# Kernel optimization log

Hardware: AMD Instinct MI355X
Metric: run time of the kernel (lower is better)

## Reference

```python
import jax, jax.numpy as jnp
import numpy as np
import math

B, SQ, SKV, H = 8, 1024, 1024, 1024
NH, HD = 16, 64  # num_attention_heads, attention_head_size


def setup_inputs() -> dict:
    key = jax.random.key(0)
    ks = jax.random.split(key, 6)
    s = 1.0 / math.sqrt(H)
    return {
        "hidden_states": jax.random.normal(ks[0], (B, SQ, H), jnp.float32),
        "keyvalue_states": jax.random.normal(ks[1], (B, SKV, H), jnp.float32),
        "attention_mask": jnp.zeros((B, 1, 1, SKV), jnp.float32),
        "Wq": jax.random.normal(ks[2], (H, H), jnp.float32) * s,
        "bq": jnp.zeros((H,), jnp.float32),
        "Wk": jax.random.normal(ks[3], (H, H), jnp.float32) * s,
        "bk": jnp.zeros((H,), jnp.float32),
        "Wv": jax.random.normal(ks[4], (H, H), jnp.float32) * s,
        "bv": jnp.zeros((H,), jnp.float32),
    }


def _split_heads(x):
    # [B, S, H] -> [B, NH, S, HD]
    b, s, _ = x.shape
    return x.reshape(b, s, NH, HD).transpose(0, 2, 1, 3)


def reference(hidden_states, keyvalue_states, attention_mask, Wq, bq, Wk, bk, Wv, bv):
    q = _split_heads(hidden_states @ Wq.T + bq)     # [B, NH, SQ, HD]
    k = _split_heads(keyvalue_states @ Wk.T + bk)   # [B, NH, SKV, HD]
    v = _split_heads(keyvalue_states @ Wv.T + bv)   # [B, NH, SKV, HD]
    scores = jnp.einsum("bhqd,bhkd->bhqk", q, k) / math.sqrt(HD)
    scores = scores + attention_mask                 # additive mask broadcast
    probs = jax.nn.softmax(scores, axis=-1)          # dropout = identity (eval)
    ctx = jnp.einsum("bhqk,bhkd->bhqd", probs, v)
    ctx = ctx.transpose(0, 2, 1, 3).reshape(hidden_states.shape[0], -1, NH * HD)
    return ctx
```

## Files before the change

### kernel.cpp

```cpp
#include <hip/hip_runtime.h>
#include <hip/hip_bf16.h>


typedef __attribute__((ext_vector_type(8))) short short8;
typedef __attribute__((ext_vector_type(4))) short short4v;
typedef __attribute__((ext_vector_type(4))) float f32x4;
typedef __attribute__((ext_vector_type(2))) float f32x2;
typedef __attribute__((ext_vector_type(16))) float f32x16;
typedef __attribute__((ext_vector_type(2))) unsigned uint2v;
typedef __attribute__((ext_vector_type(4))) int int4v;

#define AS1(p) ((const __attribute__((address_space(1))) void*)(p))
#define AS3(p) ((__attribute__((address_space(3))) void*)(p))

__device__ inline short f2bs(float x) {
    __hip_bfloat16 h = __float2bfloat16(x);
    return *reinterpret_cast<short*>(&h);
}

__global__ __launch_bounds__(256) void cvt_bf16(
    const float* __restrict__ s0, const float* __restrict__ s1,
    const float* __restrict__ s2, const float* __restrict__ s3,
    const float* __restrict__ s4,
    short* __restrict__ d0, short* __restrict__ d1,
    short* __restrict__ d2, short* __restrict__ d3, short* __restrict__ d4)
{
    const float* s; short* d; int n4;
    switch (blockIdx.y) {
        case 0: s = s0; d = d0; n4 = 2097152; break;
        case 1: s = s1; d = d1; n4 = 2097152; break;
        case 2: s = s2; d = d2; n4 = 262144;  break;
        case 3: s = s3; d = d3; n4 = 262144;  break;
        default: s = s4; d = d4; n4 = 262144; break;
    }
    for (int i = blockIdx.x * 256 + threadIdx.x; i < n4; i += gridDim.x * 256) {
        float4 v = ((const float4*)s)[i];
        short4v o;
        o.x = f2bs(v.x); o.y = f2bs(v.y); o.z = f2bs(v.z); o.w = f2bs(v.w);
        ((short4v*)d)[i] = o;
    }
}

__global__ __launch_bounds__(256) void qkv_gemm(
    const short* __restrict__ hsb, const short* __restrict__ kvb,
    const short* __restrict__ wqb, const short* __restrict__ wkb,
    const short* __restrict__ wvb,
    const float* __restrict__ bq, const float* __restrict__ bk,
    const float* __restrict__ bv,
    short* __restrict__ qo, short* __restrict__ ko, short* __restrict__ vo)
{
    const short* A; const short* W; const float* bias; short* dst;
    int z = blockIdx.z;
    if (z == 0)      { A = hsb; W = wqb; bias = bq; dst = qo; }
    else if (z == 1) { A = kvb; W = wkb; bias = bk; dst = ko; }
    else             { A = kvb; W = wvb; bias = bv; dst = vo; }

    __shared__ __align__(16) short As[128 * 64];
    __shared__ __align__(16) short Bs[128 * 64];

    const int t = threadIdx.x;
    const int lane = t & 63;
    const int wave = t >> 6;
    const int lane31 = lane & 31;
    const int hi = lane >> 5;
    const int wm = (wave & 1) * 64;
    const int wn = (wave >> 1) * 64;
    const int m0 = blockIdx.x * 128;
    const int n0 = blockIdx.y * 128;

    f32x16 acc[2][2] = {};

    for (int k0 = 0; k0 < 1024; k0 += 64) {
        #pragma unroll
        for (int i = 0; i < 4; ++i) {
            int c = i * 256 + t;
            int row = c >> 3;
            int gc = (c & 7) ^ (row & 7);
            __builtin_amdgcn_global_load_lds(
                AS1(&A[(size_t)(m0 + row) * 1024 + k0 + gc * 8]), AS3(&As[c * 8]), 16, 0, 0);
            __builtin_amdgcn_global_load_lds(
                AS1(&W[(size_t)(n0 + row) * 1024 + k0 + gc * 8]), AS3(&Bs[c * 8]), 16, 0, 0);
        }
        __syncthreads();

        #pragma unroll
        for (int kc = 0; kc < 4; ++kc) {
            short8 af[2], bf[2];
            #pragma unroll
            for (int mt = 0; mt < 2; ++mt) {
                int rr = wm + mt * 32 + lane31;
                af[mt] = *(short8*)&As[rr * 64 + ((kc * 2 + hi) ^ (rr & 7)) * 8];
            }
            #pragma unroll
            for (int nt = 0; nt < 2; ++nt) {
                int rn = wn + nt * 32 + lane31;
                bf[nt] = *(short8*)&Bs[rn * 64 + ((kc * 2 + hi) ^ (rn & 7)) * 8];
            }
            #pragma unroll
            for (int mt = 0; mt < 2; ++mt)
                #pragma unroll
                for (int nt = 0; nt < 2; ++nt)
                    acc[mt][nt] = __builtin_amdgcn_mfma_f32_32x32x16_bf16(
                        af[mt], bf[nt], acc[mt][nt], 0, 0, 0);
        }
        __syncthreads();
    }

    if (z != 2) {
        #pragma unroll
        for (int nt = 0; nt < 2; ++nt) {
            int col = n0 + wn + nt * 32 + lane31;
            float bb = bias[col];
            int h = col >> 6, d = col & 63;
            #pragma unroll
            for (int mt = 0; mt < 2; ++mt) {
                #pragma unroll
                for (int rg = 0; rg < 4; ++rg) {
                    int m = m0 + wm + mt * 32 + rg * 8 + hi * 4;
                    int b = m >> 10, s = m & 1023;
                    size_t base = (size_t)((b * 16 + h) * 1024 + s) * 64 + d;
                    #pragma unroll
                    for (int r = 0; r < 4; ++r)
                        dst[base + (size_t)r * 64] = f2bs(acc[mt][nt][rg * 4 + r] + bb);
                }
            }
        }
    } else {
        #pragma unroll
        for (int nt = 0; nt < 2; ++nt) {
            int col = n0 + wn + nt * 32 + lane31;
            float bb = bias[col];
            int h = col >> 6, d = col & 63;
            #pragma unroll
            for (int mt = 0; mt < 2; ++mt) {
                #pragma unroll
                for (int rg = 0; rg < 4; ++rg) {
                    int m = m0 + wm + mt * 32 + rg * 8 + hi * 4;
                    int b = m >> 10, s = m & 1023;
                    short4v pk;
                    pk.x = f2bs(acc[mt][nt][rg * 4 + 0] + bb);
                    pk.y = f2bs(acc[mt][nt][rg * 4 + 1] + bb);
                    pk.z = f2bs(acc[mt][nt][rg * 4 + 2] + bb);
                    pk.w = f2bs(acc[mt][nt][rg * 4 + 3] + bb);
                    *(short4v*)&dst[(size_t)((b * 16 + h) * 64 + d) * 1024 + s] = pk;
                }
            }
        }
    }
}

#define EXPC 0.18033688011112042f
#define LOG2E 1.4426950408889634f

__device__ inline uint2v half_swap(unsigned c, unsigned d, int hi) {
#if __has_builtin(__builtin_amdgcn_permlane32_swap)
    return __builtin_amdgcn_permlane32_swap(c, d, false, false);
#else
    unsigned send = hi ? c : d;
    unsigned recv = (unsigned)__shfl_xor((int)send, 32, 64);
    uint2v r;
    r.x = hi ? recv : c;
    r.y = hi ? d : recv;
    return r;
#endif
}

__device__ inline float fast_exp2(float x) {
#if __has_builtin(__builtin_amdgcn_exp2f)
    return __builtin_amdgcn_exp2f(x);
#else
    float r;
    asm("v_exp_f32 %0, %1" : "=v"(r) : "v"(x));
    return r;
#endif
}

__device__ inline unsigned cvt_pk_bf16(float a, float b) {
    unsigned r;
    asm("v_cvt_pk_bf16_f32 %0, %1, %2" : "=v"(r) : "v"(a), "v"(b));
    return r;
}

__global__ __launch_bounds__(256, 4) void attn(
    const short* __restrict__ q, const short* __restrict__ k,
    const short* __restrict__ vt, const float* __restrict__ mask,
    float* __restrict__ out)
{
    __shared__ __align__(16) short Ks[2][64 * 64];
    __shared__ __align__(16) short Vs[2][64 * 64];
    __shared__ __align__(16) float Ems[1024];

    const int t = threadIdx.x;
    const int lane = t & 63;
    const int wq = t >> 6;
    const int lane31 = lane & 31;
    const int hi = lane >> 5;

    const int id = blockIdx.x;
    const int bh = (id >> 6) * 8 + (id & 7);
    const int qt = (id >> 3) & 7;
    const int b = bh >> 4, h = bh & 15;

    const short* qbase = q + (size_t)(bh * 1024 + qt * 128) * 64;
    const short* kbase = k + (size_t)bh * 1024 * 64;
    const short* vbase = vt + (size_t)bh * 64 * 1024;

    {
        float4 mv = ((const float4*)(mask + b * 1024))[t];
        float4 o4;
        o4.x = mv.x * LOG2E; o4.y = mv.y * LOG2E;
        o4.z = mv.z * LOG2E; o4.w = mv.w * LOG2E;
        *(float4*)&Ems[t * 4] = o4;
    }

    short8 qf[4];
    #pragma unroll
    for (int kc = 0; kc < 4; ++kc)
        qf[kc] = *(const short8*)&qbase[(size_t)(wq * 32 + lane31) * 64 + kc * 16 + hi * 8];

    #pragma unroll
    for (int i = 0; i < 2; ++i) {
        int c = i * 256 + t;
        int row = c >> 3;
        int gc = (c & 7) ^ (row & 7);
        __builtin_amdgcn_global_load_lds(AS1(kbase + (size_t)row * 64 + gc * 8),
                                         AS3(&Ks[0][c * 8]), 16, 0, 0);
        __builtin_amdgcn_global_load_lds(AS1(vbase + (size_t)row * 1024 + gc * 8),
                                         AS3(&Vs[0][c * 8]), 16, 0, 0);
    }

    f32x16 o_acc[2] = {};
    f32x2 lacc = {0.f, 0.f};

    for (int kt = 0; kt < 16; ++kt) {
        __syncthreads();
        if (kt < 15) {
            int kv1 = (kt + 1) * 64;
            int nb = (kt + 1) & 1;
            #pragma unroll
            for (int i = 0; i < 2; ++i) {
                int c = i * 256 + t;
                int row = c >> 3;
                int gc = (c & 7) ^ (row & 7);
                __builtin_amdgcn_global_load_lds(
                    AS1(kbase + (size_t)(kv1 + row) * 64 + gc * 8),
                    AS3(&Ks[nb][c * 8]), 16, 0, 0);
                __builtin_amdgcn_global_load_lds(
                    AS1(vbase + (size_t)row * 1024 + kv1 + gc * 8),
                    AS3(&Vs[nb][c * 8]), 16, 0, 0);
            }
        }
        const short* ks_ = Ks[kt & 1];
        const short* vs_ = Vs[kt & 1];
        const int kv0 = kt * 64;

        f32x16 sacc[2] = {};
        #pragma unroll
        for (int kc = 0; kc < 4; ++kc) {
            #pragma unroll
            for (int mt = 0; mt < 2; ++mt) {
                int rr = mt * 32 + lane31;
                short8 ak = *(short8*)&ks_[rr * 64 + ((kc * 2 + hi) ^ (rr & 7)) * 8];
                sacc[mt] = __builtin_amdgcn_mfma_f32_32x32x16_bf16(ak, qf[kc], sacc[mt], 0, 0, 0);
            }
        }

        unsigned pk[2][4][2];
        #pragma unroll
        for (int mt = 0; mt < 2; ++mt) {
            #pragma unroll
            for (int rg = 0; rg < 4; ++rg) {
                int kvl = mt * 32 + rg * 8 + hi * 4;
                f32x4 mk = *(const f32x4*)&Ems[kv0 + kvl];
                f32x4 sv;
                sv.x = sacc[mt][rg * 4 + 0];
                sv.y = sacc[mt][rg * 4 + 1];
                sv.z = sacc[mt][rg * 4 + 2];
                sv.w = sacc[mt][rg * 4 + 3];
                f32x4 ev = sv * EXPC + mk;
                float p0 = fast_exp2(ev.x);
                float p1 = fast_exp2(ev.y);
                float p2 = fast_exp2(ev.z);
                float p3 = fast_exp2(ev.w);
                f32x2 pa; pa.x = p0; pa.y = p2;
                f32x2 pb; pb.x = p1; pb.y = p3;
                lacc += pa + pb;
                pk[mt][rg][0] = cvt_pk_bf16(p0, p1);
                pk[mt][rg][1] = cvt_pk_bf16(p2, p3);
            }
        }

        #pragma unroll
        for (int kc = 0; kc < 4; ++kc) {
            const int mt = kc >> 1, glo = (kc & 1) * 2;
            uint2v s0 = half_swap(pk[mt][glo][0], pk[mt][glo + 1][0], hi);
            uint2v s1 = half_swap(pk[mt][glo][1], pk[mt][glo + 1][1], hi);
            int4v fr; fr.x = (int)s0.x; fr.y = (int)s1.x; fr.z = (int)s0.y; fr.w = (int)s1.y;
            short8 ap = *(short8*)&fr;
            #pragma unroll
            for (int nt = 0; nt < 2; ++nt) {
                int rv = nt * 32 + lane31;
                short8 bv_ = *(short8*)&vs_[rv * 64 + ((kc * 2 + hi) ^ (rv & 7)) * 8];
                o_acc[nt] = __builtin_amdgcn_mfma_f32_32x32x16_bf16(ap, bv_, o_acc[nt], 0, 0, 0);
            }
        }
    }

    float l_sum = lacc.x + lacc.y;
    l_sum += __shfl_xor(l_sum, 32, 64);
    float invl = 1.f / l_sum;

    #pragma unroll
    for (int rg = 0; rg < 4; ++rg) {
        #pragma unroll
        for (int r = 0; r < 4; ++r) {
            int qrow_l = rg * 8 + hi * 4 + r;
            float lv = __shfl(invl, qrow_l, 64);
            int qrow = qt * 128 + wq * 32 + qrow_l;
            size_t base = (size_t)(b * 1024 + qrow) * 1024 + h * 64;
            #pragma unroll
            for (int nt = 0; nt < 2; ++nt)
                out[base + nt * 32 + lane31] = o_acc[nt][rg * 4 + r] * lv;
        }
    }
}

extern "C" void kernel_launch(void* const* d_in, const int* in_sizes, int n_in,
                              void* d_out, int out_size, void* d_ws, size_t ws_size,
                              hipStream_t stream) {
    const float* hs   = (const float*)d_in[0];
    const float* kvs  = (const float*)d_in[1];
    const float* mask = (const float*)d_in[2];
    const float* Wq   = (const float*)d_in[3];
    const float* bq   = (const float*)d_in[4];
    const float* Wk   = (const float*)d_in[5];
    const float* bk   = (const float*)d_in[6];
    const float* Wv   = (const float*)d_in[7];
    const float* bv   = (const float*)d_in[8];
    float* outp = (float*)d_out;

    const size_t big = (size_t)8 * 1024 * 1024;
    const size_t wsz = (size_t)1024 * 1024;
    short* q_ws  = (short*)d_ws;
    short* k_ws  = q_ws  + big;
    short* vt_ws = k_ws  + big;
    short* hsb   = vt_ws + big;
    short* kvb   = hsb   + big;
    short* wqb   = kvb   + big;
    short* wkb   = wqb   + wsz;
    short* wvb   = wkb   + wsz;

    cvt_bf16<<<dim3(1024, 5), 256, 0, stream>>>(hs, kvs, Wq, Wk, Wv,
                                                hsb, kvb, wqb, wkb, wvb);
    qkv_gemm<<<dim3(64, 8, 3), 256, 0, stream>>>(hsb, kvb, wqb, wkb, wvb,
                                                 bq, bk, bv, q_ws, k_ws, vt_ws);
    attn<<<dim3(1024), 256, 0, stream>>>(q_ws, k_ws, vt_ws, mask, outp);
}
```

Measured before the change: 230.7 us.

## Double-buffer QKV GEMM with 256x256 tiles and 8-wave blocks

Rewrites the QKV projection GEMM to use 256x256 output tiles with 512 threads (8 waves) and two LDS stages. The next-next K tile is prefetched with async global-to-LDS loads while the current one is being computed, and MFMA issue is bracketed by barriers and raised priority. This aims to hide global load latency and raise arithmetic intensity per tile. The cost is 128KB of LDS per block and fewer blocks (384), which risks lower occupancy and poor wave balance across the CUs.

```diff
diff --git a/kernel.cpp b/kernel.cpp
--- a/kernel.cpp
+++ b/kernel.cpp
@@ -41,7 +41,31 @@
     }
 }
 
-__global__ __launch_bounds__(256) void qkv_gemm(
+
+__device__ inline void stage8(const short* __restrict__ A,
+                              const short* __restrict__ W,
+                              short* As, short* Bs,
+                              int t, int m0, int n0, int k0)
+{
+    #pragma unroll
+    for (int i = 0; i < 4; ++i) {
+        int c = i * 512 + t;
+        int row = c >> 3;
+        int gc = (c & 7) ^ (row & 7);
+        __builtin_amdgcn_global_load_lds(
+            AS1(&A[(size_t)(m0 + row) * 1024 + k0 + gc * 8]), AS3(&As[c * 8]), 16, 0, 0);
+    }
+    #pragma unroll
+    for (int i = 0; i < 4; ++i) {
+        int c = i * 512 + t;
+        int row = c >> 3;
+        int gc = (c & 7) ^ (row & 7);
+        __builtin_amdgcn_global_load_lds(
+            AS1(&W[(size_t)(n0 + row) * 1024 + k0 + gc * 8]), AS3(&Bs[c * 8]), 16, 0, 0);
+    }
+}
+
+__global__ __launch_bounds__(512, 2) void qkv_gemm(
     const short* __restrict__ hsb, const short* __restrict__ kvb,
     const short* __restrict__ wqb, const short* __restrict__ wkb,
     const short* __restrict__ wvb,
@@ -55,68 +79,76 @@
     else if (z == 1) { A = kvb; W = wkb; bias = bk; dst = ko; }
     else             { A = kvb; W = wvb; bias = bv; dst = vo; }
 
-    __shared__ __align__(16) short As[128 * 64];
-    __shared__ __align__(16) short Bs[128 * 64];
+    __shared__ __align__(16) short As[2][256 * 64];
+    __shared__ __align__(16) short Bs[2][256 * 64];
 
     const int t = threadIdx.x;
     const int lane = t & 63;
-    const int wave = t >> 6;
+    const int wid = t >> 6;
     const int lane31 = lane & 31;
     const int hi = lane >> 5;
-    const int wm = (wave & 1) * 64;
-    const int wn = (wave >> 1) * 64;
-    const int m0 = blockIdx.x * 128;
-    const int n0 = blockIdx.y * 128;
-
-    f32x16 acc[2][2] = {};
-
-    for (int k0 = 0; k0 < 1024; k0 += 64) {
-        #pragma unroll
-        for (int i = 0; i < 4; ++i) {
-            int c = i * 256 + t;
-            int row = c >> 3;
-            int gc = (c & 7) ^ (row & 7);
-            __builtin_amdgcn_global_load_lds(
-                AS1(&A[(size_t)(m0 + row) * 1024 + k0 + gc * 8]), AS3(&As[c * 8]), 16, 0, 0);
-            __builtin_amdgcn_global_load_lds(
-                AS1(&W[(size_t)(n0 + row) * 1024 + k0 + gc * 8]), AS3(&Bs[c * 8]), 16, 0, 0);
-        }
-        __syncthreads();
+    const int wr = wid >> 2;
+    const int wc = wid & 3;
+    const int m0 = blockIdx.x * 256;
+    const int n0 = blockIdx.y * 256;
+
+    f32x16 acc[4][2] = {};
+
+    stage8(A, W, &As[0][0], &Bs[0][0], t, m0, n0, 0);
+    stage8(A, W, &As[1][0], &Bs[1][0], t, m0, n0, 64);
+
+    for (int kt = 0; kt < 16; ++kt) {
+        if (kt == 15) asm volatile("s_waitcnt vmcnt(0)" ::: "memory");
+        else          asm volatile("s_waitcnt vmcnt(8)" ::: "memory");
+        __builtin_amdgcn_s_barrier();
+
+        const short* as_ = &As[kt & 1][0];
+        const short* bs_ = &Bs[kt & 1][0];
 
         #pragma unroll
         for (int kc = 0; kc < 4; ++kc) {
-            short8 af[2], bf[2];
-            #pragma unroll
-            for (int mt = 0; mt < 2; ++mt) {
-                int rr = wm + mt * 32 + lane31;
-                af[mt] = *(short8*)&As[rr * 64 + ((kc * 2 + hi) ^ (rr & 7)) * 8];
+            short8 af[4], bf[2];
+            #pragma unroll
+            for (int mt = 0; mt < 4; ++mt) {
+                int rr = wr * 128 + mt * 32 + lane31;
+                af[mt] = *(const short8*)&as_[rr * 64 + (((kc * 2 + hi)) ^ (rr & 7)) * 8];
             }
             #pragma unroll
             for (int nt = 0; nt < 2; ++nt) {
-                int rn = wn + nt * 32 + lane31;
-                bf[nt] = *(short8*)&Bs[rn * 64 + ((kc * 2 + hi) ^ (rn & 7)) * 8];
-            }
-            #pragma unroll
-            for (int mt = 0; mt < 2; ++mt)
+                int rn = wc * 64 + nt * 32 + lane31;
+                bf[nt] = *(const short8*)&bs_[rn * 64 + (((kc * 2 + hi)) ^ (rn & 7)) * 8];
+            }
+            __builtin_amdgcn_s_barrier();
+            asm volatile("s_waitcnt lgkmcnt(0)" ::: "memory");
+            __builtin_amdgcn_sched_barrier(0);
+            __builtin_amdgcn_s_setprio(1);
+            #pragma unroll
+            for (int mt = 0; mt < 4; ++mt)
                 #pragma unroll
                 for (int nt = 0; nt < 2; ++nt)
                     acc[mt][nt] = __builtin_amdgcn_mfma_f32_32x32x16_bf16(
                         af[mt], bf[nt], acc[mt][nt], 0, 0, 0);
-        }
-        __syncthreads();
+            __builtin_amdgcn_s_setprio(0);
+            __builtin_amdgcn_s_barrier();
+        }
+
+        __builtin_amdgcn_sched_barrier(0);
+        if (kt < 14)
+            stage8(A, W, &As[kt & 1][0], &Bs[kt & 1][0], t, m0, n0, (kt + 2) * 64);
+        __builtin_amdgcn_sched_barrier(0);
     }
 
     if (z != 2) {
         #pragma unroll
         for (int nt = 0; nt < 2; ++nt) {
-            int col = n0 + wn + nt * 32 + lane31;
+            int col = n0 + wc * 64 + nt * 32 + lane31;
             float bb = bias[col];
             int h = col >> 6, d = col & 63;
             #pragma unroll
-            for (int mt = 0; mt < 2; ++mt) {
+            for (int mt = 0; mt < 4; ++mt) {
                 #pragma unroll
                 for (int rg = 0; rg < 4; ++rg) {
-                    int m = m0 + wm + mt * 32 + rg * 8 + hi * 4;
+                    int m = m0 + wr * 128 + mt * 32 + rg * 8 + hi * 4;
                     int b = m >> 10, s = m & 1023;
                     size_t base = (size_t)((b * 16 + h) * 1024 + s) * 64 + d;
                     #pragma unroll
@@ -128,14 +160,14 @@
     } else {
         #pragma unroll
         for (int nt = 0; nt < 2; ++nt) {
-            int col = n0 + wn + nt * 32 + lane31;
+            int col = n0 + wc * 64 + nt * 32 + lane31;
             float bb = bias[col];
             int h = col >> 6, d = col & 63;
             #pragma unroll
-            for (int mt = 0; mt < 2; ++mt) {
+            for (int mt = 0; mt < 4; ++mt) {
                 #pragma unroll
                 for (int rg = 0; rg < 4; ++rg) {
-                    int m = m0 + wm + mt * 32 + rg * 8 + hi * 4;
+                    int m = m0 + wr * 128 + mt * 32 + rg * 8 + hi * 4;
                     int b = m >> 10, s = m & 1023;
                     short4v pk;
                     pk.x = f2bs(acc[mt][nt][rg * 4 + 0] + bb);
@@ -352,7 +384,7 @@
 
     cvt_bf16<<<dim3(1024, 5), 256, 0, stream>>>(hs, kvs, Wq, Wk, Wv,
                                                 hsb, kvb, wqb, wkb, wvb);
-    qkv_gemm<<<dim3(64, 8, 3), 256, 0, stream>>>(hsb, kvb, wqb, wkb, wvb,
+    qkv_gemm<<<dim3(32, 4, 3), 512, 0, stream>>>(hsb, kvb, wqb, wkb, wvb,
                                                  bq, bk, bv, q_ws, k_ws, vt_ws);
     attn<<<dim3(1024), 256, 0, stream>>>(q_ws, k_ws, vt_ws, mask, outp);
 }
```

After: 260.1 us. 12.8% more time.

## Double-buffer LDS tiles in QKV GEMM to overlap global loads with MFMA

Applied to the files above, without the earlier changes.

Converts the QKV projection GEMM to a two-stage LDS pipeline. The next K tile is prefetched with global_load_lds while the current tile is consumed, using explicit vmcnt waits and barriers in place of full syncthreads. LDS use doubles to 64KB per block, and the launch bounds now ask for two blocks per CU. The aim is to hide global-memory latency behind the MFMA work. It relies on hand-counted vmcnt values, which are fragile if the number of loads changes.

```diff
diff --git a/kernel.cpp b/kernel.cpp
--- a/kernel.cpp
+++ b/kernel.cpp
@@ -41,7 +41,7 @@
     }
 }
 
-__global__ __launch_bounds__(256) void qkv_gemm(
+__global__ __launch_bounds__(256, 2) void qkv_gemm(
     const short* __restrict__ hsb, const short* __restrict__ kvb,
     const short* __restrict__ wqb, const short* __restrict__ wkb,
     const short* __restrict__ wvb,
@@ -55,8 +55,8 @@
     else if (z == 1) { A = kvb; W = wkb; bias = bk; dst = ko; }
     else             { A = kvb; W = wvb; bias = bv; dst = vo; }
 
-    __shared__ __align__(16) short As[128 * 64];
-    __shared__ __align__(16) short Bs[128 * 64];
+    __shared__ __align__(16) short As[2][128 * 64];
+    __shared__ __align__(16) short Bs[2][128 * 64];
 
     const int t = threadIdx.x;
     const int lane = t & 63;
@@ -70,18 +70,32 @@
 
     f32x16 acc[2][2] = {};
 
-    for (int k0 = 0; k0 < 1024; k0 += 64) {
+    auto STAGE = [&](int buf, int k0) {
         #pragma unroll
         for (int i = 0; i < 4; ++i) {
             int c = i * 256 + t;
             int row = c >> 3;
             int gc = (c & 7) ^ (row & 7);
             __builtin_amdgcn_global_load_lds(
-                AS1(&A[(size_t)(m0 + row) * 1024 + k0 + gc * 8]), AS3(&As[c * 8]), 16, 0, 0);
+                AS1(&A[(size_t)(m0 + row) * 1024 + k0 + gc * 8]),
+                AS3(&As[buf][c * 8]), 16, 0, 0);
             __builtin_amdgcn_global_load_lds(
-                AS1(&W[(size_t)(n0 + row) * 1024 + k0 + gc * 8]), AS3(&Bs[c * 8]), 16, 0, 0);
-        }
-        __syncthreads();
+                AS1(&W[(size_t)(n0 + row) * 1024 + k0 + gc * 8]),
+                AS3(&Bs[buf][c * 8]), 16, 0, 0);
+        }
+    };
+
+    STAGE(0, 0);
+    STAGE(1, 64);
+
+    for (int kt = 0; kt < 16; ++kt) {
+        const int cur = kt & 1;
+        if (kt == 15) asm volatile("s_waitcnt vmcnt(0)" ::: "memory");
+        else          asm volatile("s_waitcnt vmcnt(8)" ::: "memory");
+        __builtin_amdgcn_s_barrier();
+
+        const short* as_ = &As[cur][0];
+        const short* bs_ = &Bs[cur][0];
 
         #pragma unroll
         for (int kc = 0; kc < 4; ++kc) {
@@ -89,12 +103,12 @@
             #pragma unroll
             for (int mt = 0; mt < 2; ++mt) {
                 int rr = wm + mt * 32 + lane31;
-                af[mt] = *(short8*)&As[rr * 64 + ((kc * 2 + hi) ^ (rr & 7)) * 8];
+                af[mt] = *(const short8*)&as_[rr * 64 + ((kc * 2 + hi) ^ (rr & 7)) * 8];
             }
             #pragma unroll
             for (int nt = 0; nt < 2; ++nt) {
                 int rn = wn + nt * 32 + lane31;
-                bf[nt] = *(short8*)&Bs[rn * 64 + ((kc * 2 + hi) ^ (rn & 7)) * 8];
+                bf[nt] = *(const short8*)&bs_[rn * 64 + ((kc * 2 + hi) ^ (rn & 7)) * 8];
             }
             #pragma unroll
             for (int mt = 0; mt < 2; ++mt)
@@ -103,7 +117,11 @@
                     acc[mt][nt] = __builtin_amdgcn_mfma_f32_32x32x16_bf16(
                         af[mt], bf[nt], acc[mt][nt], 0, 0, 0);
         }
-        __syncthreads();
+
+        __builtin_amdgcn_sched_barrier(0);
+        __builtin_amdgcn_s_barrier();
+        if (kt < 14) STAGE(cur, (kt + 2) * 64);
+        __builtin_amdgcn_sched_barrier(0);
     }
 
     if (z != 2) {
```

New measurement: 239.2 us. 3.7% more time.

## Split QKV GEMM into Q GEMM and fused K/V GEMM sharing the A tile

Applied to the files above, without the earlier changes.

Replaces the single three-way QKV GEMM launch with a Q-only GEMM and a K/V GEMM in which each block loads the keyvalue tile once and multiplies it against both Wk and Wv tiles. This halves the A-operand global and LDS traffic for the K and V projections. The cost is twice the accumulator registers and more LDS per block in kv_gemm, which limits occupancy, plus one extra kernel launch. Both kernels gain a launch_bounds occupancy hint of 2.

```diff
diff --git a/kernel.cpp b/kernel.cpp
--- a/kernel.cpp
+++ b/kernel.cpp
@@ -41,20 +41,10 @@
     }
 }
 
-__global__ __launch_bounds__(256) void qkv_gemm(
-    const short* __restrict__ hsb, const short* __restrict__ kvb,
-    const short* __restrict__ wqb, const short* __restrict__ wkb,
-    const short* __restrict__ wvb,
-    const float* __restrict__ bq, const float* __restrict__ bk,
-    const float* __restrict__ bv,
-    short* __restrict__ qo, short* __restrict__ ko, short* __restrict__ vo)
+__global__ __launch_bounds__(256, 2) void q_gemm(
+    const short* __restrict__ hsb, const short* __restrict__ wqb,
+    const float* __restrict__ bq, short* __restrict__ qo)
 {
-    const short* A; const short* W; const float* bias; short* dst;
-    int z = blockIdx.z;
-    if (z == 0)      { A = hsb; W = wqb; bias = bq; dst = qo; }
-    else if (z == 1) { A = kvb; W = wkb; bias = bk; dst = ko; }
-    else             { A = kvb; W = wvb; bias = bv; dst = vo; }
-
     __shared__ __align__(16) short As[128 * 64];
     __shared__ __align__(16) short Bs[128 * 64];
 
@@ -77,9 +67,9 @@
             int row = c >> 3;
             int gc = (c & 7) ^ (row & 7);
             __builtin_amdgcn_global_load_lds(
-                AS1(&A[(size_t)(m0 + row) * 1024 + k0 + gc * 8]), AS3(&As[c * 8]), 16, 0, 0);
+                AS1(&hsb[(size_t)(m0 + row) * 1024 + k0 + gc * 8]), AS3(&As[c * 8]), 16, 0, 0);
             __builtin_amdgcn_global_load_lds(
-                AS1(&W[(size_t)(n0 + row) * 1024 + k0 + gc * 8]), AS3(&Bs[c * 8]), 16, 0, 0);
+                AS1(&wqb[(size_t)(n0 + row) * 1024 + k0 + gc * 8]), AS3(&Bs[c * 8]), 16, 0, 0);
         }
         __syncthreads();
 
@@ -106,44 +96,127 @@
         __syncthreads();
     }
 
-    if (z != 2) {
-        #pragma unroll
-        for (int nt = 0; nt < 2; ++nt) {
-            int col = n0 + wn + nt * 32 + lane31;
-            float bb = bias[col];
-            int h = col >> 6, d = col & 63;
+    #pragma unroll
+    for (int nt = 0; nt < 2; ++nt) {
+        int col = n0 + wn + nt * 32 + lane31;
+        float bb = bq[col];
+        int h = col >> 6, d = col & 63;
+        #pragma unroll
+        for (int mt = 0; mt < 2; ++mt) {
+            #pragma unroll
+            for (int rg = 0; rg < 4; ++rg) {
+                int m = m0 + wm + mt * 32 + rg * 8 + hi * 4;
+                int b = m >> 10, s = m & 1023;
+                size_t base = (size_t)((b * 16 + h) * 1024 + s) * 64 + d;
+                #pragma unroll
+                for (int r = 0; r < 4; ++r)
+                    qo[base + (size_t)r * 64] = f2bs(acc[mt][nt][rg * 4 + r] + bb);
+            }
+        }
+    }
+}
+
+__global__ __launch_bounds__(256, 2) void kv_gemm(
+    const short* __restrict__ kvb,
+    const short* __restrict__ wkb, const short* __restrict__ wvb,
+    const float* __restrict__ bk, const float* __restrict__ bv,
+    short* __restrict__ ko, short* __restrict__ vo)
+{
+    __shared__ __align__(16) short As[128 * 64];
+    __shared__ __align__(16) short Bk[128 * 64];
+    __shared__ __align__(16) short Bv[128 * 64];
+
+    const int t = threadIdx.x;
+    const int lane = t & 63;
+    const int wave = t >> 6;
+    const int lane31 = lane & 31;
+    const int hi = lane >> 5;
+    const int wm = (wave & 1) * 64;
+    const int wn = (wave >> 1) * 64;
+    const int m0 = blockIdx.x * 128;
+    const int n0 = blockIdx.y * 128;
+
+    f32x16 acck[2][2] = {};
+    f32x16 accv[2][2] = {};
+
+    for (int k0 = 0; k0 < 1024; k0 += 64) {
+        #pragma unroll
+        for (int i = 0; i < 4; ++i) {
+            int c = i * 256 + t;
+            int row = c >> 3;
+            int gc = (c & 7) ^ (row & 7);
+            __builtin_amdgcn_global_load_lds(
+                AS1(&kvb[(size_t)(m0 + row) * 1024 + k0 + gc * 8]), AS3(&As[c * 8]), 16, 0, 0);
+            __builtin_amdgcn_global_load_lds(
+                AS1(&wkb[(size_t)(n0 + row) * 1024 + k0 + gc * 8]), AS3(&Bk[c * 8]), 16, 0, 0);
+            __builtin_amdgcn_global_load_lds(
+                AS1(&wvb[(size_t)(n0 + row) * 1024 + k0 + gc * 8]), AS3(&Bv[c * 8]), 16, 0, 0);
+        }
+        __syncthreads();
+
+        #pragma unroll
+        for (int kc = 0; kc < 4; ++kc) {
+            short8 af[2], bfk[2], bfv[2];
             #pragma unroll
             for (int mt = 0; mt < 2; ++mt) {
+                int rr = wm + mt * 32 + lane31;
+                af[mt] = *(short8*)&As[rr * 64 + ((kc * 2 + hi) ^ (rr & 7)) * 8];
+            }
+            #pragma unroll
+            for (int nt = 0; nt < 2; ++nt) {
+                int rn = wn + nt * 32 + lane31;
+                int off = rn * 64 + ((kc * 2 + hi) ^ (rn & 7)) * 8;
+                bfk[nt] = *(short8*)&Bk[off];
+                bfv[nt] = *(short8*)&Bv[off];
+            }
+            #pragma unroll
+            for (int mt = 0; mt < 2; ++mt)
                 #pragma unroll
-                for (int rg = 0; rg < 4; ++rg) {
-                    int m = m0 + wm + mt * 32 + rg * 8 + hi * 4;
-                    int b = m >> 10, s = m & 1023;
-                    size_t base = (size_t)((b * 16 + h) * 1024 + s) * 64 + d;
-                    #pragma unroll
-                    for (int r = 0; r < 4; ++r)
-                        dst[base + (size_t)r * 64] = f2bs(acc[mt][nt][rg * 4 + r] + bb);
+                for (int nt = 0; nt < 2; ++nt) {
+                    acck[mt][nt] = __builtin_amdgcn_mfma_f32_32x32x16_bf16(
+                        af[mt], bfk[nt], acck[mt][nt], 0, 0, 0);
+                    accv[mt][nt] = __builtin_amdgcn_mfma_f32_32x32x16_bf16(
+                        af[mt], bfv[nt], accv[mt][nt], 0, 0, 0);
                 }
-            }
-        }
-    } else {
-        #pragma unroll
-        for (int nt = 0; nt < 2; ++nt) {
-            int col = n0 + wn + nt * 32 + lane31;
-            float bb = bias[col];
-            int h = col >> 6, d = col & 63;
-            #pragma unroll
-            for (int mt = 0; mt < 2; ++mt) {
+        }
+        __syncthreads();
+    }
+
+    #pragma unroll
+    for (int nt = 0; nt < 2; ++nt) {
+        int col = n0 + wn + nt * 32 + lane31;
+        float bb = bk[col];
+        int h = col >> 6, d = col & 63;
+        #pragma unroll
+        for (int mt = 0; mt < 2; ++mt) {
+            #pragma unroll
+            for (int rg = 0; rg < 4; ++rg) {
+                int m = m0 + wm + mt * 32 + rg * 8 + hi * 4;
+                int b = m >> 10, s = m & 1023;
+                size_t base = (size_t)((b * 16 + h) * 1024 + s) * 64 + d;
                 #pragma unroll
-                for (int rg = 0; rg < 4; ++rg) {
-                    int m = m0 + wm + mt * 32 + rg * 8 + hi * 4;
-                    int b = m >> 10, s = m & 1023;
-                    short4v pk;
-                    pk.x = f2bs(acc[mt][nt][rg * 4 + 0] + bb);
-                    pk.y = f2bs(acc[mt][nt][rg * 4 + 1] + bb);
-                    pk.z = f2bs(acc[mt][nt][rg * 4 + 2] + bb);
-                    pk.w = f2bs(acc[mt][nt][rg * 4 + 3] + bb);
-                    *(short4v*)&dst[(size_t)((b * 16 + h) * 64 + d) * 1024 + s] = pk;
-                }
+                for (int r = 0; r < 4; ++r)
+                    ko[base + (size_t)r * 64] = f2bs(acck[mt][nt][rg * 4 + r] + bb);
+            }
+        }
+    }
+    #pragma unroll
+    for (int nt = 0; nt < 2; ++nt) {
+        int col = n0 + wn + nt * 32 + lane31;
+        float bb = bv[col];
+        int h = col >> 6, d = col & 63;
+        #pragma unroll
+        for (int mt = 0; mt < 2; ++mt) {
+            #pragma unroll
+            for (int rg = 0; rg < 4; ++rg) {
+                int m = m0 + wm + mt * 32 + rg * 8 + hi * 4;
+                int b = m >> 10, s = m & 1023;
+                short4v pk;
+                pk.x = f2bs(accv[mt][nt][rg * 4 + 0] + bb);
+                pk.y = f2bs(accv[mt][nt][rg * 4 + 1] + bb);
+                pk.z = f2bs(accv[mt][nt][rg * 4 + 2] + bb);
+                pk.w = f2bs(accv[mt][nt][rg * 4 + 3] + bb);
+                *(short4v*)&vo[(size_t)((b * 16 + h) * 64 + d) * 1024 + s] = pk;
             }
         }
     }
@@ -352,7 +425,7 @@
 
     cvt_bf16<<<dim3(1024, 5), 256, 0, stream>>>(hs, kvs, Wq, Wk, Wv,
                                                 hsb, kvb, wqb, wkb, wvb);
-    qkv_gemm<<<dim3(64, 8, 3), 256, 0, stream>>>(hsb, kvb, wqb, wkb, wvb,
-                                                 bq, bk, bv, q_ws, k_ws, vt_ws);
+    q_gemm<<<dim3(64, 8), 256, 0, stream>>>(hsb, wqb, bq, q_ws);
+    kv_gemm<<<dim3(64, 8), 256, 0, stream>>>(kvb, wkb, wvb, bk, bv, k_ws, vt_ws);
     attn<<<dim3(1024), 256, 0, stream>>>(q_ws, k_ws, vt_ws, mask, outp);
 }
```

Result: no change. 230.4 us (-0.1%).
